# Performance work log

Hardware: AMD Instinct MI355X
Metric: run time of the kernel (lower is better)

## Reference

```python
import jax, jax.numpy as jnp
import numpy as np

DIM = 128
GRID = 8
RED = 16  # LCBAM channel-attention reduction
B, L = 16, 4096


def setup_inputs() -> dict:
    key = jax.random.key(0)
    ks = jax.random.split(key, 8)
    scale = 1.0 / (np.sqrt(DIM) * np.sqrt(GRID))
    return {
        "x": jax.random.normal(ks[0], (B, L, DIM), jnp.float32),
        "n1_g": jnp.ones((DIM,), jnp.float32),
        "n1_b": jnp.zeros((DIM,), jnp.float32),
        "fk1_c": jax.random.normal(ks[1], (2, DIM, DIM, GRID), jnp.float32) * scale,
        "fk1_b": jnp.zeros((DIM,), jnp.float32),
        "n2_g": jnp.ones((DIM,), jnp.float32),
        "n2_b": jnp.zeros((DIM,), jnp.float32),
        "fk2_c": jax.random.normal(ks[2], (2, DIM, DIM, GRID), jnp.float32) * scale,
        "fk2_b": jnp.zeros((DIM,), jnp.float32),
        "w1": jax.random.normal(ks[3], (DIM // RED, DIM), jnp.float32) * 0.05,  # channel-MLP reduce
        "w2": jax.random.normal(ks[4], (DIM, DIM // RED), jnp.float32) * 0.05,  # channel-MLP expand
        "conv_w": jax.random.normal(ks[5], (1, 2, 7, 7), jnp.float32) * 0.05,   # spatial-attn 7x7 conv
    }


def _layernorm(x, g, b, eps=1e-5):
    m = jnp.mean(x, axis=-1, keepdims=True)
    v = jnp.var(x, axis=-1, keepdims=True)
    return (x - m) * jax.lax.rsqrt(v + eps) * g + b


def _fkan(x, coeffs, bias):
    # x: (B,L,I); coeffs: (2,O,I,G)
    k = jnp.arange(1, GRID + 1, dtype=x.dtype)          # (G,)
    ang = x[..., None] * k                               # (B,L,I,G)
    y = jnp.einsum("blig,oig->blo", jnp.cos(ang), coeffs[0])
    y = y + jnp.einsum("blig,oig->blo", jnp.sin(ang), coeffs[1])
    return y + bias


def reference(x, n1_g, n1_b, fk1_c, fk1_b, n2_g, n2_b, fk2_c, fk2_b, w1, w2, conv_w):
    residual = x
    out = _fkan(_layernorm(x, n1_g, n1_b), fk1_c, fk1_b)
    out = jax.nn.relu(out)
    out = _fkan(_layernorm(out, n2_g, n2_b), fk2_c, fk2_b)
    b, l, c = out.shape
    x4 = out.reshape(b, c, 1, l)  # faithful to torch .view (raw reshape, not transpose)
    # LCBAM channel attention: avg+max pool -> shared MLP -> sigmoid
    avg = jnp.mean(x4, axis=(2, 3))   # (B,C)
    mx = jnp.max(x4, axis=(2, 3))     # (B,C)
    mlp = lambda v: jax.nn.relu(v @ w1.T) @ w2.T
    ca = jax.nn.sigmoid(mlp(avg) + mlp(mx))[:, :, None, None]
    x4 = x4 * ca
    # LCBAM spatial attention: channel mean/max -> 7x7 conv -> sigmoid
    s_in = jnp.concatenate([jnp.mean(x4, axis=1, keepdims=True),
                            jnp.max(x4, axis=1, keepdims=True)], axis=1)  # (B,2,1,L)
    sa = jax.lax.conv_general_dilated(s_in, conv_w, (1, 1), ((3, 3), (3, 3)))
    x4 = x4 * jax.nn.sigmoid(sa)
    out = x4.reshape(b, l, c)
    return residual + out
```

## Files before the change

kernel.cpp:

```cpp
#include <hip/hip_runtime.h>
#include <math.h>

typedef unsigned short ushort_t;
typedef unsigned int uint_t;
typedef _Float16 half_t;

#define DIMC 128
#define NB 16
#define NL 4096

using f32x4 = __attribute__((ext_vector_type(4))) float;
using bf16x8 = __attribute__((ext_vector_type(8))) short;
using half4 = __attribute__((ext_vector_type(4))) half_t;

__device__ __forceinline__ ushort_t bf16rne(float f) {
  uint_t b = __float_as_uint(f);
  b += 0x7fffu + ((b >> 16) & 1u);
  return (ushort_t)(b >> 16);
}

__device__ __forceinline__ uint_t pkbf(float lo, float hi) {
  union { __bf16 h[2]; uint_t u; } u;
  u.h[0] = (__bf16)lo;
  u.h[1] = (__bf16)hi;
  return u.u;
}

__device__ __forceinline__ float bf2f(ushort_t u) {
  return __uint_as_float(((uint_t)u) << 16);
}

__global__ __launch_bounds__(256) void prep_coef_k(const float* __restrict__ fk1,
                                                   const float* __restrict__ fk2,
                                                   ushort_t* __restrict__ coefT) {
  int idx = blockIdx.x * 256 + threadIdx.x;
  int layer = idx >> 15;
  int rem = idx & 32767;
  int ci = rem >> 11;
  int n = (rem >> 8) & 7;
  int s = (rem >> 6) & 3;
  int l = rem & 63;
  int o = n * 16 + (l & 15);
  int kbase = ci * 128 + s * 32 + (l >> 4) * 8;
  const float* src = layer ? fk2 : fk1;
  uint_t p[4];
#pragma unroll
  for (int jj = 0; jj < 4; ++jj) {
    int k0 = kbase + jj * 2;
    int t0 = k0 & 1, g0 = (k0 >> 1) & 7, i0 = k0 >> 4;
    int k1 = k0 + 1;
    int t1 = k1 & 1, g1 = (k1 >> 1) & 7, i1 = k1 >> 4;
    ushort_t a = bf16rne(src[((t0 * DIMC + o) * DIMC + i0) * 8 + g0]);
    ushort_t b = bf16rne(src[((t1 * DIMC + o) * DIMC + i1) * 8 + g1]);
    p[jj] = (uint_t)a | ((uint_t)b << 16);
  }
  uint4 w;
  w.x = p[0]; w.y = p[1]; w.z = p[2]; w.w = p[3];
  *(uint4*)&coefT[idx * 8] = w;
}

constexpr int SXH = 132;

__global__ __launch_bounds__(256, 2) void fkan_main_k(
    const float* __restrict__ x,
    const float* __restrict__ n1g, const float* __restrict__ n1b,
    const float* __restrict__ fk1b,
    const float* __restrict__ n2g, const float* __restrict__ n2b,
    const float* __restrict__ fk2b,
    const ushort_t* __restrict__ coefT,
    ushort_t* __restrict__ out2,
    float* __restrict__ chanSum, float* __restrict__ chanMax) {

  __shared__ half_t xln[128 * SXH];
  __shared__ uint4 feat[4][2][2][64];

  const int tid = threadIdx.x;
  const int bid = blockIdx.x;
  const int lane = tid & 63;
  const int wid = tid >> 6;
  const int rowBase = wid * 32;
  const size_t tileBase = (size_t)bid * 128 * DIMC;

  {
    const float4* src = (const float4*)(x + tileBase + (size_t)rowBase * DIMC);
#pragma unroll
    for (int j = 0; j < 16; ++j) {
      int idx = j * 64 + lane;
      float4 v = src[idx];
      half4 h;
      h.x = (half_t)v.x; h.y = (half_t)v.y; h.z = (half_t)v.z; h.w = (half_t)v.w;
      *(half4*)&xln[(rowBase + (idx >> 5)) * SXH + (idx & 31) * 4] = h;
    }
  }

  auto layernorm = [&](const float* gg, const float* bb) {
    float g0 = gg[lane], g1 = gg[lane + 64];
    float be0 = bb[lane], be1 = bb[lane + 64];
#pragma unroll
    for (int j = 0; j < 32; ++j) {
      int t = rowBase + j;
      float v0 = (float)xln[t * SXH + lane], v1 = (float)xln[t * SXH + 64 + lane];
      float s = v0 + v1, q = v0 * v0 + v1 * v1;
#pragma unroll
      for (int m = 1; m < 64; m <<= 1) {
        s += __shfl_xor(s, m, 64);
        q += __shfl_xor(q, m, 64);
      }
      float mean = s * (1.0f / DIMC);
      float var = q * (1.0f / DIMC) - mean * mean;
      float rr = rsqrtf(var + 1e-5f);
      xln[t * SXH + lane] = (half_t)((v0 - mean) * rr * g0 + be0);
      xln[t * SXH + 64 + lane] = (half_t)((v1 - mean) * rr * g1 + be1);
    }
  };

  layernorm(n1g, n1b);

  const int tl = lane & 31;
  const int chOff = lane >> 5;
  const int mmw = tl >> 4;
  const int l0 = (tl & 15) + (chOff << 5);
  const half_t* xch = &xln[(rowBase + tl) * SXH + chOff];

  auto chain_gen = [&](int chunk, int ns, int nbuf) {
    float a = (float)xch[chunk * 8 + ns * 2];
    float s1, c1;
    __sincosf(a, &s1, &c1);
    uint_t q0 = pkbf(c1, s1);
    float ck = c1, sk = s1, cn, sn;
    cn = ck * c1 - sk * s1; sn = sk * c1 + ck * s1; ck = cn; sk = sn;
    uint_t q1 = pkbf(ck, sk);
    cn = ck * c1 - sk * s1; sn = sk * c1 + ck * s1; ck = cn; sk = sn;
    uint_t q2 = pkbf(ck, sk);
    cn = ck * c1 - sk * s1; sn = sk * c1 + ck * s1; ck = cn; sk = sn;
    uint_t q3 = pkbf(ck, sk);
    cn = ck * c1 - sk * s1; sn = sk * c1 + ck * s1; ck = cn; sk = sn;
    uint_t q4 = pkbf(ck, sk);
    cn = ck * c1 - sk * s1; sn = sk * c1 + ck * s1; ck = cn; sk = sn;
    uint_t q5 = pkbf(ck, sk);
    cn = ck * c1 - sk * s1; sn = sk * c1 + ck * s1; ck = cn; sk = sn;
    uint_t q6 = pkbf(ck, sk);
    cn = ck * c1 - sk * s1; sn = sk * c1 + ck * s1; ck = cn; sk = sn;
    uint_t q7 = pkbf(ck, sk);
    uint4 w0; w0.x = q0; w0.y = q1; w0.z = q2; w0.w = q3;
    uint4 w1; w1.x = q4; w1.y = q5; w1.z = q6; w1.w = q7;
    feat[wid][nbuf][mmw][l0] = w0;
    feat[wid][nbuf][mmw][l0 + 16] = w1;
  };

  f32x4 acc[8][2];

  auto ldBs = [&](const ushort_t* cbase, int step, bf16x8 (&bf)[8]) {
    int ci = (step >> 2) & 15, s = step & 3;
#pragma unroll
    for (int nn = 0; nn < 8; ++nn)
      bf[nn] = *(const bf16x8*)(cbase +
          (size_t)((((ci * 8 + nn) * 4 + s) << 6) + lane) * 8);
  };

  auto mfma16 = [&](bf16x8 a0, bf16x8 a1, bf16x8 (&bf)[8]) {
    __builtin_amdgcn_s_setprio(1);
#pragma unroll
    for (int nn = 0; nn < 8; ++nn) {
      acc[nn][0] = __builtin_amdgcn_mfma_f32_16x16x32_bf16(a0, bf[nn],
                                                           acc[nn][0], 0, 0, 0);
      acc[nn][1] = __builtin_amdgcn_mfma_f32_16x16x32_bf16(a1, bf[nn],
                                                           acc[nn][1], 0, 0, 0);
    }
    __builtin_amdgcn_s_setprio(0);
  };

  auto run_layer = [&](const ushort_t* cbase) {
#pragma unroll
    for (int nn = 0; nn < 8; ++nn)
#pragma unroll
      for (int mm = 0; mm < 2; ++mm) acc[nn][mm] = (f32x4)(0.f);
    bf16x8 bfE[8], bfO[8];
    ldBs(cbase, 0, bfE);
    chain_gen(0, 0, 0);
#pragma unroll 1
    for (int it = 0; it < 32; ++it) {
      const int e = it * 2;
      ldBs(cbase, e + 1, bfO);
      chain_gen(((e + 1) >> 2) & 15, (e + 1) & 3, 1);
      {
        bf16x8 a0 = *(const bf16x8*)&feat[wid][0][0][lane];
        bf16x8 a1 = *(const bf16x8*)&feat[wid][0][1][lane];
        mfma16(a0, a1, bfE);
      }
      ldBs(cbase, e + 2, bfE);
      chain_gen(((e + 2) >> 2) & 15, (e + 2) & 3, 0);
      {
        bf16x8 a0 = *(const bf16x8*)&feat[wid][1][0][lane];
        bf16x8 a1 = *(const bf16x8*)&feat[wid][1][1][lane];
        mfma16(a0, a1, bfO);
      }
    }
  };

  run_layer(coefT);

#pragma unroll
  for (int nn = 0; nn < 8; ++nn) {
    int o = nn * 16 + (lane & 15);
    float bia = fk1b[o];
#pragma unroll
    for (int mm = 0; mm < 2; ++mm) {
      int trow = rowBase + mm * 16 + (lane >> 4) * 4;
#pragma unroll
      for (int r = 0; r < 4; ++r)
        xln[(trow + r) * SXH + o] = (half_t)fmaxf(acc[nn][mm][r] + bia, 0.f);
    }
  }

  layernorm(n2g, n2b);

  run_layer(coefT + 262144);

  float ls = 0.f, lm = -INFINITY;
#pragma unroll
  for (int nn = 0; nn < 8; ++nn) {
    int o = nn * 16 + (lane & 15);
    float bia = fk2b[o];
#pragma unroll
    for (int mm = 0; mm < 2; ++mm) {
      int trow = rowBase + mm * 16 + (lane >> 4) * 4;
#pragma unroll
      for (int r = 0; r < 4; ++r) {
        float v = acc[nn][mm][r] + bia;
        out2[tileBase + (size_t)(trow + r) * DIMC + o] = bf16rne(v);
        ls += v;
        lm = fmaxf(lm, v);
      }
    }
  }
#pragma unroll
  for (int m = 1; m < 64; m <<= 1) {
    ls += __shfl_xor(ls, m, 64);
    lm = fmaxf(lm, __shfl_xor(lm, m, 64));
  }
  if (lane == 0) {
    chanSum[bid * 4 + wid] = ls;
    chanMax[bid * 4 + wid] = lm;
  }
}

__global__ __launch_bounds__(128) void tail_k(
    const float* __restrict__ x, const ushort_t* __restrict__ out2,
    const float* __restrict__ chanSum, const float* __restrict__ chanMax,
    const float* __restrict__ w1, const float* __restrict__ w2,
    const float* __restrict__ convw, float* __restrict__ dout) {
  int b = blockIdx.x >> 5;
  int t = blockIdx.x & 31;
  int c = threadIdx.x;
  __shared__ float avs[DIMC], mxs[DIMC], hh[16], cas[DIMC];
  __shared__ float sM[134], sX[134];

  avs[c] = chanSum[b * DIMC + c] * (1.0f / NL);
  mxs[c] = chanMax[b * DIMC + c];
  __syncthreads();
  if (c < 16) {
    const float* v = (c < 8) ? avs : mxs;
    float a = 0.f;
    for (int i = 0; i < DIMC; ++i) a += v[i] * w1[(c & 7) * DIMC + i];
    hh[c] = fmaxf(a, 0.f);
  }
  __syncthreads();
  {
    float z = 0.f;
#pragma unroll
    for (int r = 0; r < 8; ++r) z += (hh[r] + hh[8 + r]) * w2[c * 8 + r];
    cas[c] = 1.0f / (1.0f + expf(-z));
  }
  __syncthreads();

  const ushort_t* o2b = out2 + (size_t)b * NL * DIMC;
  float s = 0.f, m = -INFINITY;
#pragma unroll 4
  for (int c4 = 0; c4 < 128; ++c4) {
    float v = bf2f(o2b[(size_t)(c4 * 32 + t) * DIMC + c]) * cas[c4];
    s += v;
    m = fmaxf(m, v);
  }
  sM[c + 3] = s * (1.0f / DIMC);
  sX[c + 3] = m;
  if (c < 6) {
    bool left = c < 3;
    int tp = left ? t - 1 : t + 1;
    int cc = left ? 125 + c : c - 3;
    int di = left ? c : 131 + (c - 3);
    float ss = 0.f, mm2 = -INFINITY;
    if (tp >= 0 && tp < 32) {
#pragma unroll 4
      for (int c4 = 0; c4 < 128; ++c4) {
        float v = bf2f(o2b[(size_t)(c4 * 32 + tp) * DIMC + cc]) * cas[c4];
        ss += v;
        mm2 = fmaxf(mm2, v);
      }
      sM[di] = ss * (1.0f / DIMC);
      sX[di] = mm2;
    } else {
      sM[di] = 0.f;
      sX[di] = 0.f;
    }
  }
  __syncthreads();

  float sa = 0.f;
#pragma unroll
  for (int d = 0; d < 7; ++d)
    sa += convw[21 + d] * sM[c + d] + convw[70 + d] * sX[c + d];
  float sig = 1.0f / (1.0f + expf(-sa));

  const float* xb = x + (size_t)b * NL * DIMC;
  float* db = dout + (size_t)b * NL * DIMC;
#pragma unroll 2
  for (int c4 = 0; c4 < 128; ++c4) {
    size_t idx = (size_t)(c4 * 32 + t) * DIMC + c;
    db[idx] = xb[idx] + bf2f(o2b[idx]) * cas[c4] * sig;
  }
}

extern "C" void kernel_launch(void* const* d_in, const int* in_sizes, int n_in,
                              void* d_out, int out_size, void* d_ws, size_t ws_size,
                              hipStream_t stream) {
  const float* x = (const float*)d_in[0];
  const float* n1g = (const float*)d_in[1];
  const float* n1b = (const float*)d_in[2];
  const float* fk1c = (const float*)d_in[3];
  const float* fk1b = (const float*)d_in[4];
  const float* n2g = (const float*)d_in[5];
  const float* n2b = (const float*)d_in[6];
  const float* fk2c = (const float*)d_in[7];
  const float* fk2b = (const float*)d_in[8];
  const float* w1 = (const float*)d_in[9];
  const float* w2 = (const float*)d_in[10];
  const float* convw = (const float*)d_in[11];

  ushort_t* out2 = (ushort_t*)d_ws;
  ushort_t* coefT = out2 + 8388608;
  float* chanSum = (float*)(coefT + 524288);
  float* chanMax = chanSum + 2048;
  float* dout = (float*)d_out;

  prep_coef_k<<<256, 256, 0, stream>>>(fk1c, fk2c, coefT);
  fkan_main_k<<<512, 256, 0, stream>>>(x, n1g, n1b, fk1b, n2g, n2b,
                                       fk2b, coefT, out2, chanSum, chanMax);
  tail_k<<<NB * 32, 128, 0, stream>>>(x, out2, chanSum, chanMax, w1, w2, convw, dout);
}
```

Before: 158.0 us.

## Use Chebyshev recurrence for Fourier features and restructure coefficient prefetch

Replaces the rotation-based harmonic chain (four multiplies per step) with a Chebyshev recurrence that needs one multiply-subtract per sine and cosine term. The base sin/cos now comes from hardware sin/cos intrinsics on a range-reduced argument. The B-fragment loads change from a two-deep register double buffer to a single buffer loaded in the same step, and angle values are prefetched two steps ahead from LDS. This cuts ALU work and register pressure, but coefficient loads are now less hidden, and the Chebyshev recurrence may accumulate more rounding error.

Result: faster. 145.1 us (-8.2%).

```diff
diff --git a/kernel.cpp b/kernel.cpp
--- a/kernel.cpp
+++ b/kernel.cpp
@@ -122,28 +122,29 @@
   const int l0 = (tl & 15) + (chOff << 5);
   const half_t* xch = &xln[(rowBase + tl) * SXH + chOff];
 
-  auto chain_gen = [&](int chunk, int ns, int nbuf) {
-    float a = (float)xch[chunk * 8 + ns * 2];
-    float s1, c1;
-    __sincosf(a, &s1, &c1);
-    uint_t q0 = pkbf(c1, s1);
-    float ck = c1, sk = s1, cn, sn;
-    cn = ck * c1 - sk * s1; sn = sk * c1 + ck * s1; ck = cn; sk = sn;
-    uint_t q1 = pkbf(ck, sk);
-    cn = ck * c1 - sk * s1; sn = sk * c1 + ck * s1; ck = cn; sk = sn;
-    uint_t q2 = pkbf(ck, sk);
-    cn = ck * c1 - sk * s1; sn = sk * c1 + ck * s1; ck = cn; sk = sn;
-    uint_t q3 = pkbf(ck, sk);
-    cn = ck * c1 - sk * s1; sn = sk * c1 + ck * s1; ck = cn; sk = sn;
-    uint_t q4 = pkbf(ck, sk);
-    cn = ck * c1 - sk * s1; sn = sk * c1 + ck * s1; ck = cn; sk = sn;
-    uint_t q5 = pkbf(ck, sk);
-    cn = ck * c1 - sk * s1; sn = sk * c1 + ck * s1; ck = cn; sk = sn;
-    uint_t q6 = pkbf(ck, sk);
-    cn = ck * c1 - sk * s1; sn = sk * c1 + ck * s1; ck = cn; sk = sn;
-    uint_t q7 = pkbf(ck, sk);
-    uint4 w0; w0.x = q0; w0.y = q1; w0.z = q2; w0.w = q3;
-    uint4 w1; w1.x = q4; w1.y = q5; w1.z = q6; w1.w = q7;
+  auto angAt = [&](int step) -> float {
+    return (float)xch[((step >> 2) & 15) * 8 + (step & 3) * 2];
+  };
+
+  auto chain_cheb = [&](float a, int nbuf) {
+    float r = a * 0.15915494309189535f;
+    r = r - floorf(r);
+    float s1 = __builtin_amdgcn_sinf(r);
+    float c1 = __builtin_amdgcn_cosf(r);
+    float tc = c1 + c1;
+    float c2 = tc * c1 - 1.0f;
+    float s2 = tc * s1;
+    float c3 = tc * c2 - c1, s3 = tc * s2 - s1;
+    float c4 = tc * c3 - c2, s4 = tc * s3 - s2;
+    float c5 = tc * c4 - c3, s5 = tc * s4 - s3;
+    float c6 = tc * c5 - c4, s6 = tc * s5 - s4;
+    float c7 = tc * c6 - c5, s7 = tc * s6 - s5;
+    float c8 = tc * c7 - c6, s8 = tc * s7 - s6;
+    uint4 w0, w1;
+    w0.x = pkbf(c1, s1); w0.y = pkbf(c2, s2);
+    w0.z = pkbf(c3, s3); w0.w = pkbf(c4, s4);
+    w1.x = pkbf(c5, s5); w1.y = pkbf(c6, s6);
+    w1.z = pkbf(c7, s7); w1.w = pkbf(c8, s8);
     feat[wid][nbuf][mmw][l0] = w0;
     feat[wid][nbuf][mmw][l0 + 16] = w1;
   };
@@ -175,25 +176,31 @@
     for (int nn = 0; nn < 8; ++nn)
 #pragma unroll
       for (int mm = 0; mm < 2; ++mm) acc[nn][mm] = (f32x4)(0.f);
-    bf16x8 bfE[8], bfO[8];
-    ldBs(cbase, 0, bfE);
-    chain_gen(0, 0, 0);
+    chain_cheb(angAt(0), 0);
+    float aP1 = angAt(1);
+    float aP2 = angAt(2);
 #pragma unroll 1
     for (int it = 0; it < 32; ++it) {
       const int e = it * 2;
-      ldBs(cbase, e + 1, bfO);
-      chain_gen(((e + 1) >> 2) & 15, (e + 1) & 3, 1);
       {
+        bf16x8 bf[8];
+        ldBs(cbase, e, bf);
+        float aN = angAt(e + 3);
+        chain_cheb(aP1, 1);
         bf16x8 a0 = *(const bf16x8*)&feat[wid][0][0][lane];
         bf16x8 a1 = *(const bf16x8*)&feat[wid][0][1][lane];
-        mfma16(a0, a1, bfE);
-      }
-      ldBs(cbase, e + 2, bfE);
-      chain_gen(((e + 2) >> 2) & 15, (e + 2) & 3, 0);
+        mfma16(a0, a1, bf);
+        aP1 = aP2; aP2 = aN;
+      }
       {
+        bf16x8 bf[8];
+        ldBs(cbase, e + 1, bf);
+        float aN = angAt(e + 4);
+        chain_cheb(aP1, 0);
         bf16x8 a0 = *(const bf16x8*)&feat[wid][1][0][lane];
         bf16x8 a1 = *(const bf16x8*)&feat[wid][1][1][lane];
-        mfma16(a0, a1, bfO);
+        mfma16(a0, a1, bf);
+        aP1 = aP2; aP2 = aN;
       }
     }
   };
```
